# Kernel optimization log

Measured on AMD Instinct MI355X. Metric: run time of the kernel, lower is better.

Reference implementation:

```python
import jax, jax.numpy as jnp
import numpy as np

N_NODES = 50000
N_EDGES = 800000
IN_CH = 128
HID = 64
HEADS = 4
OUT_CH = 10
NUM_GRAPHS = 500
NEG_SLOPE = 0.2  # PyG GATConv default LeakyReLU slope


def gat_conv(x, src, dst, W, a_src, a_dst, b, concat):
    """One PyG-style GATConv (inference; attention dropout disabled).
    x: [N, F_in], src/dst: [E'] (self-loops already appended).
    W: [F_in, H*C], a_src/a_dst: [H, C], b: [H*C] or [C].
    """
    N = x.shape[0]
    H, C = a_src.shape
    h = (x @ W).reshape(N, H, C)                      # [N,H,C]
    al_s = jnp.einsum('nhc,hc->nh', h, a_src)          # [N,H]
    al_d = jnp.einsum('nhc,hc->nh', h, a_dst)          # [N,H]
    e = al_s[src] + al_d[dst]                          # [E,H]
    e = jnp.where(e > 0, e, NEG_SLOPE * e)             # leaky_relu
    # segment softmax over edges sharing the same destination node
    e_max = jax.ops.segment_max(e, dst, num_segments=N)
    ex = jnp.exp(e - e_max[dst])
    denom = jax.ops.segment_sum(ex, dst, num_segments=N)
    alpha = ex / (denom[dst] + 1e-16)                  # [E,H]
    msg = h[src] * alpha[:, :, None]                   # [E,H,C]
    out = jax.ops.segment_sum(msg, dst, num_segments=N)  # [N,H,C]
    out = out.reshape(N, H * C) if concat else out.mean(axis=1)
    return out + b


def _forward(x, edge_index, batch, W1, a_src1, a_dst1, b1,
             W2, a_src2, a_dst2, b2, fc_w, fc_b):
    N = x.shape[0]
    loops = jnp.arange(N, dtype=edge_index.dtype)
    src = jnp.concatenate([edge_index[0], loops])
    dst = jnp.concatenate([edge_index[1], loops])
    h = gat_conv(x, src, dst, W1, a_src1, a_dst1, b1, concat=True)
    h = jax.nn.relu(h)                                  # dropout: eval mode
    h = gat_conv(h, src, dst, W2, a_src2, a_dst2, b2, concat=False)
    pooled = jax.ops.segment_sum(h, batch, num_segments=NUM_GRAPHS)  # global_add_pool
    logits = pooled @ fc_w + fc_b
    return jax.nn.log_softmax(logits, axis=1)


def setup_inputs() -> dict:
    key = jax.random.key(0)
    ks = jax.random.split(key, 12)
    g = lambda k, shp, fan: jax.random.normal(k, shp, dtype=jnp.float32) * (1.0 / np.sqrt(fan))
    x = jax.random.normal(ks[0], (N_NODES, IN_CH), dtype=jnp.float32)
    edge_index = jax.random.randint(ks[1], (2, N_EDGES), 0, N_NODES, dtype=jnp.int64)
    batch = jnp.sort(jax.random.randint(ks[2], (N_NODES,), 0, NUM_GRAPHS, dtype=jnp.int64))
    return {
        'x': x,
        'edge_index': edge_index,
        'batch': batch,
        'W1': g(ks[3], (IN_CH, HEADS * HID), IN_CH),
        'a_src1': g(ks[4], (HEADS, HID), HID),
        'a_dst1': g(ks[5], (HEADS, HID), HID),
        'b1': jnp.zeros((HEADS * HID,), dtype=jnp.float32),
        'W2': g(ks[6], (HEADS * HID, HID), HEADS * HID),
        'a_src2': g(ks[7], (1, HID), HID),
        'a_dst2': g(ks[8], (1, HID), HID),
        'b2': jnp.zeros((HID,), dtype=jnp.float32),
        'fc_w': g(ks[9], (HID, OUT_CH), HID),
        'fc_b': jnp.zeros((OUT_CH,), dtype=jnp.float32),
    }


def reference(x, edge_index, batch, W1, a_src1, a_dst1, b1,
              W2, a_src2, a_dst2, b2, fc_w, fc_b):
    return _forward(x, edge_index, batch, W1, a_src1, a_dst1, b1,
                    W2, a_src2, a_dst2, b2, fc_w, fc_b)
```

## Files before the change

### kernel.cpp

```cpp
#include <hip/hip_runtime.h>
#include <hip/hip_fp16.h>
#include <math.h>

#define N_NODES   50000
#define N_EDGES   800000
#define IN_CH     128
#define HID       64
#define HEADS     4
#define F1        (HEADS * HID)
#define OUT_CH    10
#define NUM_GRAPHS 500
#define NEG_SLOPE 0.2f
#define RPAD      132
#define NTILES    (N_NODES / 16)
#define CAP       64

typedef __attribute__((ext_vector_type(8))) _Float16 half8;
typedef __attribute__((ext_vector_type(4))) float floatx4;

__device__ __forceinline__ unsigned short f2h(float f) {
    _Float16 h = (_Float16)f;
    unsigned short u; __builtin_memcpy(&u, &h, 2); return u;
}
__device__ __forceinline__ unsigned int pack_h2(float lo, float hi) {
    auto r = __builtin_amdgcn_cvt_pkrtz(lo, hi);
    unsigned int u; __builtin_memcpy(&u, &r, 4); return u;
}
__device__ __forceinline__ float h2f(unsigned short u) {
    _Float16 h; __builtin_memcpy(&h, &u, 2); return (float)h;
}

__global__ void init_kernel(int* __restrict__ cnt, unsigned short* __restrict__ csr,
                            const float* __restrict__ W1, unsigned short* __restrict__ W1p,
                            const float* __restrict__ W2, unsigned short* __restrict__ W2p)
{
    const int gid = blockIdx.x * blockDim.x + threadIdx.x;
    if (gid < N_NODES) {
        cnt[gid] = 1;
        csr[gid * CAP] = (unsigned short)gid;
    }
    if (gid < 4096) {
        const int t = gid >> 8, kt = (gid >> 6) & 3, l = gid & 63;
        const int col = t * 16 + (l & 15);
        unsigned short* o = W1p + (size_t)((t * 4 + kt) * 64 + l) * 8;
        #pragma unroll
        for (int j = 0; j < 8; ++j) {
            const int k = kt * 32 + (l >> 4) * 8 + j;
            o[j] = f2h(W1[k * F1 + col]);
        }
    } else if (gid < 6144) {
        const int g2 = gid - 4096;
        const int t = g2 >> 9, kt = (g2 >> 6) & 7, l = g2 & 63;
        const int col = t * 16 + (l & 15);
        unsigned short* o = W2p + (size_t)((t * 8 + kt) * 64 + l) * 8;
        #pragma unroll
        for (int j = 0; j < 8; ++j) {
            const int k = kt * 32 + (l >> 4) * 8 + j;
            o[j] = f2h(W2[k * HID + col]);
        }
    }
}

__global__ __launch_bounds__(256) void scatter_gemm1(
    const int* __restrict__ ei, int* __restrict__ cnt,
    unsigned short* __restrict__ csr,
    const float* __restrict__ x, const unsigned short* __restrict__ W1p,
    const float* __restrict__ a_src1, const float* __restrict__ a_dst1,
    unsigned short* __restrict__ H1b,
    float* __restrict__ al_s1, float* __restrict__ al_d1)
{
    const int e = blockIdx.x * 256 + threadIdx.x;
    const int src = ei[e];
    const int dst = ei[N_EDGES + e];
    const int slot = atomicAdd(&cnt[dst], 1);

    const int m0 = blockIdx.x * 16;
    const int w = threadIdx.x >> 6;
    const int l = threadIdx.x & 63;
    const int q = l >> 4, r = l & 15;
    floatx4 acc[4] = {};
    const float* arow = x + (size_t)(m0 + r) * IN_CH + q * 8;
    #pragma unroll
    for (int kt = 0; kt < 4; ++kt) {
        const float4 f0 = *(const float4*)(arow + kt * 32);
        const float4 f1 = *(const float4*)(arow + kt * 32 + 4);
        union { uint4 u; half8 h; } a;
        a.u = make_uint4(pack_h2(f0.x, f0.y), pack_h2(f0.z, f0.w),
                         pack_h2(f1.x, f1.y), pack_h2(f1.z, f1.w));
        #pragma unroll
        for (int t = 0; t < 4; ++t) {
            const int nt = w * 4 + t;
            const half8 b = *(const half8*)(W1p + (size_t)((nt * 4 + kt) * 64 + l) * 8);
            acc[t] = __builtin_amdgcn_mfma_f32_16x16x32_f16(a.h, b, acc[t], 0, 0, 0);
        }
    }
    float ls[4] = {0.f, 0.f, 0.f, 0.f}, ld[4] = {0.f, 0.f, 0.f, 0.f};
    #pragma unroll
    for (int t = 0; t < 4; ++t) {
        const int col = (w * 4 + t) * 16 + r;
        const float as = a_src1[col], ad = a_dst1[col];
        #pragma unroll
        for (int reg = 0; reg < 4; ++reg) {
            H1b[(size_t)(m0 + q * 4 + reg) * F1 + col] = f2h(acc[t][reg]);
            ls[reg] += acc[t][reg] * as;
            ld[reg] += acc[t][reg] * ad;
        }
    }
    #pragma unroll
    for (int reg = 0; reg < 4; ++reg) {
        #pragma unroll
        for (int off = 8; off > 0; off >>= 1) {
            ls[reg] += __shfl_down(ls[reg], off, 16);
            ld[reg] += __shfl_down(ld[reg], off, 16);
        }
    }
    if (r == 0) {
        #pragma unroll
        for (int reg = 0; reg < 4; ++reg) {
            const int n = m0 + q * 4 + reg;
            al_s1[n * HEADS + w] = ls[reg];
            al_d1[n * HEADS + w] = ld[reg];
        }
    }

    if (slot < CAP) csr[dst * CAP + slot] = (unsigned short)src;
}

__global__ __launch_bounds__(256) void agg1_gemm2(
    const int* __restrict__ cnt, const unsigned short* __restrict__ csr,
    const float* __restrict__ al_s1, const float* __restrict__ al_d1,
    const uint2* __restrict__ H1b2, const float* __restrict__ b1,
    const unsigned short* __restrict__ W2p,
    const float* __restrict__ a_src2, const float* __restrict__ a_dst2,
    unsigned short* __restrict__ H2b,
    float* __restrict__ al_s2, float* __restrict__ al_d2)
{
    const int m0 = blockIdx.x * 16;
    const int w = threadIdx.x >> 6;
    const int l = threadIdx.x & 63;
    const char* H1base = (const char*)H1b2;
    __shared__ unsigned int rows[16][RPAD];
    __shared__ unsigned int sofs[16][CAP];
    __shared__ uint2        wtp[16][CAP];

    int nreg[4];
    #pragma unroll
    for (int d = 0; d < 4; ++d) {
        const int dd = w * 4 + d;
        const int dstn = m0 + dd;
        const int n = min(cnt[dstn], CAP);
        nreg[d] = n;
        const float4 ad = *(const float4*)(al_d1 + dstn * 4);
        float w0 = 0.f, w1 = 0.f, w2 = 0.f, w3 = 0.f;
        unsigned int off = 0;
        if (l < n) {
            const int s = csr[dstn * CAP + l];
            off = (unsigned int)s << 9;
            const float4 as = *(const float4*)(al_s1 + s * 4);
            float t0 = as.x + ad.x; t0 = t0 > 0.f ? t0 : NEG_SLOPE * t0;
            float t1 = as.y + ad.y; t1 = t1 > 0.f ? t1 : NEG_SLOPE * t1;
            float t2 = as.z + ad.z; t2 = t2 > 0.f ? t2 : NEG_SLOPE * t2;
            float t3 = as.w + ad.w; t3 = t3 > 0.f ? t3 : NEG_SLOPE * t3;
            w0 = __expf(t0); w1 = __expf(t1); w2 = __expf(t2); w3 = __expf(t3);
        }
        sofs[dd][l] = off;
        wtp[dd][l] = make_uint2(pack_h2(w0, w1), pack_h2(w2, w3));
    }
    __syncthreads();

    const int hf = l >> 5;
    const int ll = l & 31;
    const int hh = ll >> 3;
    const unsigned int lane16 = (unsigned int)(ll * 16);
    const float4 bb0 = *(const float4*)(b1 + 8 * ll);
    const float4 bb4 = *(const float4*)(b1 + 8 * ll + 4);
    #pragma unroll 1
    for (int d = 0; d < 4; ++d) {
        const int dd = w * 4 + d;
        const int n = nreg[d];
        float a0=0.f,a1=0.f,a2=0.f,a3=0.f,a4=0.f,a5=0.f,a6=0.f,a7=0.f,den=0.f;
        const int n8 = (n + 7) & ~7;
        for (int i = 0; i < n8; i += 8) {
            unsigned int off[4]; float wt[4];
            #pragma unroll
            for (int j = 0; j < 4; ++j) {
                const int slot = i + 2 * j + hf;
                off[j] = sofs[dd][slot];
                const uint2 wp = wtp[dd][slot];
                const unsigned int uw = (hh & 2) ? wp.y : wp.x;
                wt[j] = h2f((hh & 1) ? (unsigned short)(uw >> 16)
                                     : (unsigned short)(uw & 0xFFFFu));
            }
            uint4 u[4];
            #pragma unroll
            for (int j = 0; j < 4; ++j)
                u[j] = *(const uint4*)(H1base + (off[j] + lane16));
            #pragma unroll
            for (int j = 0; j < 4; ++j) {
                union { uint4 v; _Float16 hv[8]; } c; c.v = u[j];
                a0 += wt[j] * (float)c.hv[0];
                a1 += wt[j] * (float)c.hv[1];
                a2 += wt[j] * (float)c.hv[2];
                a3 += wt[j] * (float)c.hv[3];
                a4 += wt[j] * (float)c.hv[4];
                a5 += wt[j] * (float)c.hv[5];
                a6 += wt[j] * (float)c.hv[6];
                a7 += wt[j] * (float)c.hv[7];
                den += wt[j];
            }
        }
        a0 += __shfl_xor(a0, 32, 64);
        a1 += __shfl_xor(a1, 32, 64);
        a2 += __shfl_xor(a2, 32, 64);
        a3 += __shfl_xor(a3, 32, 64);
        a4 += __shfl_xor(a4, 32, 64);
        a5 += __shfl_xor(a5, 32, 64);
        a6 += __shfl_xor(a6, 32, 64);
        a7 += __shfl_xor(a7, 32, 64);
        den += __shfl_xor(den, 32, 64);
        if (l < 32) {
            const float rcp = 1.f / (den + 1e-16f);
            float v0 = fmaxf(a0 * rcp + bb0.x, 0.f);
            float v1 = fmaxf(a1 * rcp + bb0.y, 0.f);
            float v2 = fmaxf(a2 * rcp + bb0.z, 0.f);
            float v3 = fmaxf(a3 * rcp + bb0.w, 0.f);
            float v4 = fmaxf(a4 * rcp + bb4.x, 0.f);
            float v5 = fmaxf(a5 * rcp + bb4.y, 0.f);
            float v6 = fmaxf(a6 * rcp + bb4.z, 0.f);
            float v7 = fmaxf(a7 * rcp + bb4.w, 0.f);
            *(uint4*)&rows[dd][4 * ll] = make_uint4(pack_h2(v0, v1), pack_h2(v2, v3),
                                                    pack_h2(v4, v5), pack_h2(v6, v7));
        }
    }
    __syncthreads();

    const int q = l >> 4, r = l & 15;
    floatx4 acc = {};
    #pragma unroll
    for (int kt = 0; kt < 8; ++kt) {
        union { uint4 u; half8 hh2; } a;
        a.u = *(const uint4*)&rows[r][kt * 16 + q * 4];
        const half8 b = *(const half8*)(W2p + (size_t)((w * 8 + kt) * 64 + l) * 8);
        acc = __builtin_amdgcn_mfma_f32_16x16x32_f16(a.hh2, b, acc, 0, 0, 0);
    }
    const int col = w * 16 + r;
    const float as = a_src2[col], ad2 = a_dst2[col];
    float ls[4], ld[4];
    #pragma unroll
    for (int reg = 0; reg < 4; ++reg) {
        H2b[(size_t)(m0 + q * 4 + reg) * HID + col] = f2h(acc[reg]);
        ls[reg] = acc[reg] * as;
        ld[reg] = acc[reg] * ad2;
    }
    #pragma unroll
    for (int reg = 0; reg < 4; ++reg) {
        #pragma unroll
        for (int off = 8; off > 0; off >>= 1) {
            ls[reg] += __shfl_down(ls[reg], off, 16);
            ld[reg] += __shfl_down(ld[reg], off, 16);
        }
    }
    __shared__ float Ls[4][16], Ld[4][16];
    if (r == 0) {
        #pragma unroll
        for (int reg = 0; reg < 4; ++reg) {
            Ls[w][q * 4 + reg] = ls[reg];
            Ld[w][q * 4 + reg] = ld[reg];
        }
    }
    __syncthreads();
    if (threadIdx.x < 16) {
        const int row = threadIdx.x;
        al_s2[m0 + row] = Ls[0][row] + Ls[1][row] + Ls[2][row] + Ls[3][row];
        al_d2[m0 + row] = Ld[0][row] + Ld[1][row] + Ld[2][row] + Ld[3][row];
    }
}

__global__ __launch_bounds__(256) void agg2_csr(
    const int* __restrict__ cnt, const unsigned short* __restrict__ csr,
    const float* __restrict__ al_s2, const float* __restrict__ al_d2,
    const uint4* __restrict__ H2b4, uint4* __restrict__ out2b4)
{
    const int dst = blockIdx.x * 4 + (threadIdx.x >> 6);
    const int l = threadIdx.x & 63;
    const int oct = l >> 3, j = l & 7;
    const int n = min(cnt[dst], CAP);
    const float ad = al_d2[dst];
    float a0=0.f,a1=0.f,a2=0.f,a3=0.f,a4=0.f,a5=0.f,a6=0.f,a7=0.f,den=0.f;
    int s_reg = 0;
    float w_reg = 0.f;
    if (l < n) {
        s_reg = csr[dst * CAP + l];
        float t = al_s2[s_reg] + ad;
        t = t > 0.f ? t : NEG_SLOPE * t;
        w_reg = __expf(t);
    }
    const int n32 = (n + 31) & ~31;
    for (int i = 0; i < n32; i += 32) {
        int   srcs[4]; float wts[4];
        #pragma unroll
        for (int k = 0; k < 4; ++k) {
            const int e = i + 8 * k + oct;
            srcs[k] = __shfl(s_reg, e, 64);
            wts[k]  = __shfl(w_reg, e, 64);
        }
        uint4 u[4];
        #pragma unroll
        for (int k = 0; k < 4; ++k)
            u[k] = H2b4[(size_t)srcs[k] * (HID / 8) + j];
        #pragma unroll
        for (int k = 0; k < 4; ++k) {
            union { uint4 v; _Float16 hv[8]; } c; c.v = u[k];
            a0 += wts[k] * (float)c.hv[0];
            a1 += wts[k] * (float)c.hv[1];
            a2 += wts[k] * (float)c.hv[2];
            a3 += wts[k] * (float)c.hv[3];
            a4 += wts[k] * (float)c.hv[4];
            a5 += wts[k] * (float)c.hv[5];
            a6 += wts[k] * (float)c.hv[6];
            a7 += wts[k] * (float)c.hv[7];
            den += wts[k];
        }
    }
    #pragma unroll
    for (int m = 8; m <= 32; m <<= 1) {
        a0 += __shfl_xor(a0, m, 64);
        a1 += __shfl_xor(a1, m, 64);
        a2 += __shfl_xor(a2, m, 64);
        a3 += __shfl_xor(a3, m, 64);
        a4 += __shfl_xor(a4, m, 64);
        a5 += __shfl_xor(a5, m, 64);
        a6 += __shfl_xor(a6, m, 64);
        a7 += __shfl_xor(a7, m, 64);
        den += __shfl_xor(den, m, 64);
    }
    if (l < 8) {
        const float rcp = 1.f / (den + 1e-16f);
        out2b4[(size_t)dst * (HID / 8) + j] =
            make_uint4(pack_h2(a0 * rcp, a1 * rcp), pack_h2(a2 * rcp, a3 * rcp),
                       pack_h2(a4 * rcp, a5 * rcp), pack_h2(a6 * rcp, a7 * rcp));
    }
}

__global__ __launch_bounds__(256) void pool_fc_kernel(
    const unsigned short* __restrict__ out2b, const float* __restrict__ b2,
    const int* __restrict__ batch,
    const float* __restrict__ fc_w, const float* __restrict__ fc_b,
    float* __restrict__ out)
{
    const int g = blockIdx.x;
    const int q = threadIdx.x >> 6, c = threadIdx.x & 63;
    __shared__ int se[2];
    __shared__ float partial[4][HID];
    __shared__ float pl[HID];
    __shared__ float logits[OUT_CH];
    if (threadIdx.x < 2) {
        const int target = g + threadIdx.x;
        int lo = 0, hi = N_NODES;
        while (lo < hi) { int mid = (lo + hi) >> 1; if (batch[mid] < target) lo = mid + 1; else hi = mid; }
        se[threadIdx.x] = lo;
    }
    __syncthreads();
    const int start = se[0], end = se[1];
    float acc = 0.f;
    for (int n = start + q; n < end; n += 4)
        acc += h2f(out2b[(size_t)n * HID + c]);
    partial[q][c] = acc;
    __syncthreads();
    if (q == 0)
        pl[c] = partial[0][c] + partial[1][c] + partial[2][c] + partial[3][c]
              + (float)(end - start) * b2[c];
    __syncthreads();
    if (threadIdx.x < OUT_CH) {
        float lg = fc_b[threadIdx.x];
        #pragma unroll
        for (int k = 0; k < HID; ++k) lg += pl[k] * fc_w[k * OUT_CH + threadIdx.x];
        logits[threadIdx.x] = lg;
    }
    __syncthreads();
    if (threadIdx.x == 0) {
        float m = logits[0];
        #pragma unroll
        for (int j2 = 1; j2 < OUT_CH; ++j2) m = fmaxf(m, logits[j2]);
        float s = 0.f;
        #pragma unroll
        for (int j2 = 0; j2 < OUT_CH; ++j2) s += __expf(logits[j2] - m);
        const float lse = m + __logf(s);
        #pragma unroll
        for (int j2 = 0; j2 < OUT_CH; ++j2) out[g * OUT_CH + j2] = logits[j2] - lse;
    }
}


extern "C" void kernel_launch(void* const* d_in, const int* in_sizes, int n_in,
                              void* d_out, int out_size, void* d_ws, size_t ws_size,
                              hipStream_t stream)
{
    const float* x      = (const float*)d_in[0];
    const int*   ei     = (const int*)  d_in[1];
    const int*   batch  = (const int*)  d_in[2];
    const float* W1     = (const float*)d_in[3];
    const float* a_src1 = (const float*)d_in[4];
    const float* a_dst1 = (const float*)d_in[5];
    const float* b1     = (const float*)d_in[6];
    const float* W2     = (const float*)d_in[7];
    const float* a_src2 = (const float*)d_in[8];
    const float* a_dst2 = (const float*)d_in[9];
    const float* b2     = (const float*)d_in[10];
    const float* fc_w   = (const float*)d_in[11];
    const float* fc_b   = (const float*)d_in[12];
    float* out = (float*)d_out;

    char* ws = (char*)d_ws;
    size_t off = 0;
    auto alloc_b = [&](size_t bytes) { void* p = (void*)(ws + off); off += (bytes + 15) & ~15ull; return p; };

    unsigned short* H1b  = (unsigned short*)alloc_b((size_t)N_NODES * F1 * 2);
    float* al_s1  = (float*)alloc_b((size_t)N_NODES * HEADS * 4);
    float* al_d1  = (float*)alloc_b((size_t)N_NODES * HEADS * 4);
    unsigned short* H2b  = (unsigned short*)alloc_b((size_t)N_NODES * HID * 2);
    float* al_s2  = (float*)alloc_b((size_t)N_NODES * 4);
    float* al_d2  = (float*)alloc_b((size_t)N_NODES * 4);
    unsigned short* out2b = (unsigned short*)alloc_b((size_t)N_NODES * HID * 2);
    int*   cnt    = (int*)alloc_b((size_t)N_NODES * 4);
    unsigned short* csr = (unsigned short*)alloc_b((size_t)N_NODES * CAP * 2);
    unsigned short* W1p = (unsigned short*)alloc_b((size_t)IN_CH * F1 * 2);
    unsigned short* W2p = (unsigned short*)alloc_b((size_t)F1 * HID * 2);

    init_kernel<<<(N_NODES + 255) / 256, 256, 0, stream>>>(cnt, csr, W1, W1p, W2, W2p);

    scatter_gemm1<<<NTILES, 256, 0, stream>>>(ei, cnt, csr, x, W1p,
                                              a_src1, a_dst1, H1b, al_s1, al_d1);

    agg1_gemm2<<<N_NODES / 16, 256, 0, stream>>>(cnt, csr, al_s1, al_d1,
                                                 (const uint2*)H1b, b1,
                                                 W2p, a_src2, a_dst2,
                                                 H2b, al_s2, al_d2);

    agg2_csr<<<N_NODES / 4, 256, 0, stream>>>(cnt, csr, al_s2, al_d2,
                                              (const uint4*)H2b, (uint4*)out2b);

    pool_fc_kernel<<<NUM_GRAPHS, 256, 0, stream>>>(out2b, b2, batch, fc_w, fc_b, out);
}
```

Before: 234.8 us.

## Fuse layer-2 aggregation into per-graph pooling kernel

Merges the second GAT aggregation with global add pooling and the FC/log-softmax, so each graph's block aggregates its own nodes and accumulates pooled features in registers. This removes the intermediate fp16 node-output buffer write/read and one kernel launch. In exchange, the grid shrinks to one 512-thread block per graph, so far fewer waves are available to hide gather latency, and load balance depends on graph sizes.

```diff
diff --git a/kernel.cpp b/kernel.cpp
--- a/kernel.cpp
+++ b/kernel.cpp
@@ -276,82 +276,20 @@
     }
 }
 
-__global__ __launch_bounds__(256) void agg2_csr(
+__global__ __launch_bounds__(512) void agg2_pool(
     const int* __restrict__ cnt, const unsigned short* __restrict__ csr,
     const float* __restrict__ al_s2, const float* __restrict__ al_d2,
-    const uint4* __restrict__ H2b4, uint4* __restrict__ out2b4)
-{
-    const int dst = blockIdx.x * 4 + (threadIdx.x >> 6);
-    const int l = threadIdx.x & 63;
-    const int oct = l >> 3, j = l & 7;
-    const int n = min(cnt[dst], CAP);
-    const float ad = al_d2[dst];
-    float a0=0.f,a1=0.f,a2=0.f,a3=0.f,a4=0.f,a5=0.f,a6=0.f,a7=0.f,den=0.f;
-    int s_reg = 0;
-    float w_reg = 0.f;
-    if (l < n) {
-        s_reg = csr[dst * CAP + l];
-        float t = al_s2[s_reg] + ad;
-        t = t > 0.f ? t : NEG_SLOPE * t;
-        w_reg = __expf(t);
-    }
-    const int n32 = (n + 31) & ~31;
-    for (int i = 0; i < n32; i += 32) {
-        int   srcs[4]; float wts[4];
-        #pragma unroll
-        for (int k = 0; k < 4; ++k) {
-            const int e = i + 8 * k + oct;
-            srcs[k] = __shfl(s_reg, e, 64);
-            wts[k]  = __shfl(w_reg, e, 64);
-        }
-        uint4 u[4];
-        #pragma unroll
-        for (int k = 0; k < 4; ++k)
-            u[k] = H2b4[(size_t)srcs[k] * (HID / 8) + j];
-        #pragma unroll
-        for (int k = 0; k < 4; ++k) {
-            union { uint4 v; _Float16 hv[8]; } c; c.v = u[k];
-            a0 += wts[k] * (float)c.hv[0];
-            a1 += wts[k] * (float)c.hv[1];
-            a2 += wts[k] * (float)c.hv[2];
-            a3 += wts[k] * (float)c.hv[3];
-            a4 += wts[k] * (float)c.hv[4];
-            a5 += wts[k] * (float)c.hv[5];
-            a6 += wts[k] * (float)c.hv[6];
-            a7 += wts[k] * (float)c.hv[7];
-            den += wts[k];
-        }
-    }
-    #pragma unroll
-    for (int m = 8; m <= 32; m <<= 1) {
-        a0 += __shfl_xor(a0, m, 64);
-        a1 += __shfl_xor(a1, m, 64);
-        a2 += __shfl_xor(a2, m, 64);
-        a3 += __shfl_xor(a3, m, 64);
-        a4 += __shfl_xor(a4, m, 64);
-        a5 += __shfl_xor(a5, m, 64);
-        a6 += __shfl_xor(a6, m, 64);
-        a7 += __shfl_xor(a7, m, 64);
-        den += __shfl_xor(den, m, 64);
-    }
-    if (l < 8) {
-        const float rcp = 1.f / (den + 1e-16f);
-        out2b4[(size_t)dst * (HID / 8) + j] =
-            make_uint4(pack_h2(a0 * rcp, a1 * rcp), pack_h2(a2 * rcp, a3 * rcp),
-                       pack_h2(a4 * rcp, a5 * rcp), pack_h2(a6 * rcp, a7 * rcp));
-    }
-}
-
-__global__ __launch_bounds__(256) void pool_fc_kernel(
-    const unsigned short* __restrict__ out2b, const float* __restrict__ b2,
+    const uint4* __restrict__ H2b4, const float* __restrict__ b2,
     const int* __restrict__ batch,
     const float* __restrict__ fc_w, const float* __restrict__ fc_b,
     float* __restrict__ out)
 {
     const int g = blockIdx.x;
-    const int q = threadIdx.x >> 6, c = threadIdx.x & 63;
+    const int w = threadIdx.x >> 6;
+    const int l = threadIdx.x & 63;
+    const int oct = l >> 3, j = l & 7;
     __shared__ int se[2];
-    __shared__ float partial[4][HID];
+    __shared__ float partial[8][HID];
     __shared__ float pl[HID];
     __shared__ float logits[OUT_CH];
     if (threadIdx.x < 2) {
@@ -362,14 +300,77 @@
     }
     __syncthreads();
     const int start = se[0], end = se[1];
-    float acc = 0.f;
-    for (int n = start + q; n < end; n += 4)
-        acc += h2f(out2b[(size_t)n * HID + c]);
-    partial[q][c] = acc;
-    __syncthreads();
-    if (q == 0)
-        pl[c] = partial[0][c] + partial[1][c] + partial[2][c] + partial[3][c]
-              + (float)(end - start) * b2[c];
+
+    float pacc[8] = {};
+    for (int dst = start + w; dst < end; dst += 8) {
+        const int n = min(cnt[dst], CAP);
+        const float ad = al_d2[dst];
+        float a0=0.f,a1=0.f,a2=0.f,a3=0.f,a4=0.f,a5=0.f,a6=0.f,a7=0.f,den=0.f;
+        int s_reg = 0;
+        float w_reg = 0.f;
+        if (l < n) {
+            s_reg = csr[dst * CAP + l];
+            float t = al_s2[s_reg] + ad;
+            t = t > 0.f ? t : NEG_SLOPE * t;
+            w_reg = __expf(t);
+        }
+        const int n32 = (n + 31) & ~31;
+        for (int i = 0; i < n32; i += 32) {
+            int   srcs[4]; float wts[4];
+            #pragma unroll
+            for (int k = 0; k < 4; ++k) {
+                const int e = i + 8 * k + oct;
+                srcs[k] = __shfl(s_reg, e, 64);
+                wts[k]  = __shfl(w_reg, e, 64);
+            }
+            uint4 u[4];
+            #pragma unroll
+            for (int k = 0; k < 4; ++k)
+                u[k] = H2b4[(size_t)srcs[k] * (HID / 8) + j];
+            #pragma unroll
+            for (int k = 0; k < 4; ++k) {
+                union { uint4 v; _Float16 hv[8]; } c; c.v = u[k];
+                a0 += wts[k] * (float)c.hv[0];
+                a1 += wts[k] * (float)c.hv[1];
+                a2 += wts[k] * (float)c.hv[2];
+                a3 += wts[k] * (float)c.hv[3];
+                a4 += wts[k] * (float)c.hv[4];
+                a5 += wts[k] * (float)c.hv[5];
+                a6 += wts[k] * (float)c.hv[6];
+                a7 += wts[k] * (float)c.hv[7];
+                den += wts[k];
+            }
+        }
+        #pragma unroll
+        for (int m = 8; m <= 32; m <<= 1) {
+            a0 += __shfl_xor(a0, m, 64);
+            a1 += __shfl_xor(a1, m, 64);
+            a2 += __shfl_xor(a2, m, 64);
+            a3 += __shfl_xor(a3, m, 64);
+            a4 += __shfl_xor(a4, m, 64);
+            a5 += __shfl_xor(a5, m, 64);
+            a6 += __shfl_xor(a6, m, 64);
+            a7 += __shfl_xor(a7, m, 64);
+            den += __shfl_xor(den, m, 64);
+        }
+        const float rcp = 1.f / (den + 1e-16f);
+        pacc[0] += a0 * rcp; pacc[1] += a1 * rcp;
+        pacc[2] += a2 * rcp; pacc[3] += a3 * rcp;
+        pacc[4] += a4 * rcp; pacc[5] += a5 * rcp;
+        pacc[6] += a6 * rcp; pacc[7] += a7 * rcp;
+    }
+    if (oct == 0) {
+        #pragma unroll
+        for (int p = 0; p < 8; ++p) partial[w][8 * j + p] = pacc[p];
+    }
+    __syncthreads();
+    if (threadIdx.x < HID) {
+        const int c = threadIdx.x;
+        float s = (float)(end - start) * b2[c];
+        #pragma unroll
+        for (int ww = 0; ww < 8; ++ww) s += partial[ww][c];
+        pl[c] = s;
+    }
     __syncthreads();
     if (threadIdx.x < OUT_CH) {
         float lg = fc_b[threadIdx.x];
@@ -421,7 +422,6 @@
     unsigned short* H2b  = (unsigned short*)alloc_b((size_t)N_NODES * HID * 2);
     float* al_s2  = (float*)alloc_b((size_t)N_NODES * 4);
     float* al_d2  = (float*)alloc_b((size_t)N_NODES * 4);
-    unsigned short* out2b = (unsigned short*)alloc_b((size_t)N_NODES * HID * 2);
     int*   cnt    = (int*)alloc_b((size_t)N_NODES * 4);
     unsigned short* csr = (unsigned short*)alloc_b((size_t)N_NODES * CAP * 2);
     unsigned short* W1p = (unsigned short*)alloc_b((size_t)IN_CH * F1 * 2);
@@ -437,8 +437,7 @@
                                                  W2p, a_src2, a_dst2,
                                                  H2b, al_s2, al_d2);
 
-    agg2_csr<<<N_NODES / 4, 256, 0, stream>>>(cnt, csr, al_s2, al_d2,
-                                              (const uint4*)H2b, (uint4*)out2b);
-
-    pool_fc_kernel<<<NUM_GRAPHS, 256, 0, stream>>>(out2b, b2, batch, fc_w, fc_b, out);
-}
+    agg2_pool<<<NUM_GRAPHS, 512, 0, stream>>>(cnt, csr, al_s2, al_d2,
+                                              (const uint4*)H2b, b2, batch,
+                                              fc_w, fc_b, out);
+}
```

Result: no change. 236.4 us (+0.7%).
